# Performance work log

Measured on AMD Instinct MI355X. Metric: run time of the kernel, lower is better.

## Reference

```python
import jax, jax.numpy as jnp
import numpy as np

NUM_HEADS = 16

def setup_inputs() -> dict:
    key = jax.random.key(0)
    k1, k2, k3 = jax.random.split(key, 3)
    B, N, C = 2, 2048, 1024
    x = jax.random.normal(k1, (B, N, C), dtype=jnp.float32)
    w_qkv = jax.random.normal(k2, (C, 3 * C), dtype=jnp.float32) * (C ** -0.5)
    w_proj = jax.random.normal(k3, (C, C), dtype=jnp.float32) * (C ** -0.5)
    b_proj = jnp.zeros((C,), dtype=jnp.float32)
    return {"x": x, "w_qkv": w_qkv, "w_proj": w_proj, "b_proj": b_proj}

def reference(x, w_qkv, w_proj, b_proj):
    B, N, C = x.shape
    H = NUM_HEADS
    D = C // H
    scale = D ** -0.5
    qkv = (x @ w_qkv).reshape(B, N, 3, H, D).transpose(2, 0, 3, 1, 4)  # [3,B,H,N,D]
    q, k, v = qkv[0], qkv[1], qkv[2]
    attn = jnp.einsum("bhnd,bhmd->bhnm", q, k) * scale  # [B,H,N,N]
    attn = jax.nn.softmax(attn, axis=-1)
    out = jnp.einsum("bhnm,bhmd->bhnd", attn, v)  # [B,H,N,D]
    out = out.transpose(0, 2, 1, 3).reshape(B, N, C)
    return out @ w_proj + b_proj
```

## Files before the change

kernel.cpp:

```cpp
#include <hip/hip_runtime.h>
#include <hip/hip_bf16.h>
#include <math.h>

#define B_SZ   2
#define N_SEQ  2048
#define C_DIM  1024
#define H_NUM  16
#define D_HEAD 64
#define M_ROWS (B_SZ * N_SEQ)
#define QKV_N  (3 * C_DIM)

typedef __attribute__((ext_vector_type(8))) short  bf16x8;
typedef __attribute__((ext_vector_type(4))) float  floatx4;

static __device__ __forceinline__ unsigned short f2bf(float x) {
    unsigned int u = __float_as_uint(x);
    u = (u + 0x7FFFu + ((u >> 16) & 1u)) >> 16;
    return (unsigned short)u;
}
static __device__ __forceinline__ unsigned int f2bf_hi(float x) {
    unsigned int u = __float_as_uint(x);
    return u + 0x7FFFu + ((u >> 16) & 1u);
}
#if __has_builtin(__builtin_amdgcn_cvt_pk_bf16_f32)
typedef __bf16 bf16_2 __attribute__((ext_vector_type(2)));
static __device__ __forceinline__ unsigned int pkbf(float a, float b) {
    union { bf16_2 v; unsigned int u; } c;
    c.v = __builtin_amdgcn_cvt_pk_bf16_f32(a, b);
    return c.u;
}
#else
static __device__ __forceinline__ unsigned int pkbf(float a, float b) {
    return __builtin_amdgcn_perm(f2bf_hi(b), f2bf_hi(a), 0x07060302u);
}
#endif

#if __has_builtin(__builtin_amdgcn_exp2f)
#define EXP2F(x) __builtin_amdgcn_exp2f(x)
#else
#define EXP2F(x) exp2f(x)
#endif

#define GLP(p) ((const __attribute__((address_space(1))) void*)(p))
#define LDP(p) ((__attribute__((address_space(3))) void*)(p))

#define CEXP 0.18033688011112042f

__global__ __launch_bounds__(256)
void prep_fused(const float* __restrict__ x,      unsigned short* __restrict__ xb,
                const float* __restrict__ w_qkv,  unsigned short* __restrict__ wqkvT,
                const float* __restrict__ w_proj, unsigned short* __restrict__ wprojT)
{
    __shared__ unsigned short t[64][72];
    const int bid = blockIdx.x;
    const int tid = threadIdx.x;

    if (bid < 4096) {
        const int i = bid * 256 + tid;
        float4 v = ((const float4*)x)[i];
        ushort4 p;
        p.x = f2bf(v.x); p.y = f2bf(v.y); p.z = f2bf(v.z); p.w = f2bf(v.w);
        ((ushort4*)xb)[i] = p;
        return;
    }

    const float* W;
    unsigned short* WT;
    int N, tt;
    if (bid < 4096 + 768) { W = w_qkv;  WT = wqkvT;  N = QKV_N; tt = bid - 4096; }
    else                  { W = w_proj; WT = wprojT; N = C_DIM; tt = bid - 4864; }
    const int ntiles = N / 64;
    const int n0 = (tt % ntiles) * 64;
    const int k0 = (tt / ntiles) * 64;
    const int K  = C_DIM;

    const int tc = tid & 15;
    const int tr = tid >> 4;
    #pragma unroll
    for (int p = 0; p < 4; ++p) {
        const int r = tr + p * 16;
        float4 v = *(const float4*)&W[(size_t)(k0 + r) * N + n0 + tc * 4];
        ushort4 pk;
        pk.x = f2bf(v.x); pk.y = f2bf(v.y); pk.z = f2bf(v.z); pk.w = f2bf(v.w);
        *(ushort4*)&t[r][tc * 4] = pk;
    }
    __syncthreads();

    const int n  = tid >> 2;
    const int c0 = (tid & 3) * 16;
    unsigned short tmp[16];
    #pragma unroll
    for (int i = 0; i < 16; ++i) tmp[i] = t[c0 + i][n];
    *(uint4*)&WT[(size_t)(n0 + n) * K + k0 + c0]     = *(uint4*)&tmp[0];
    *(uint4*)&WT[(size_t)(n0 + n) * K + k0 + c0 + 8] = *(uint4*)&tmp[8];
}

__global__ __launch_bounds__(256)
void gemm_qkv(const unsigned short* __restrict__ A,
              const unsigned short* __restrict__ BT,
              unsigned short* __restrict__ qbuf,
              unsigned short* __restrict__ kbuf,
              unsigned short* __restrict__ vbuf)
{
    const int K = C_DIM;
    __shared__ unsigned short As[128 * 64];
    __shared__ unsigned short Bs[128 * 64];

    const int tid  = threadIdx.x;
    const int lane = tid & 63;
    const int wave = tid >> 6;
    const int l15  = lane & 15;
    const int lq   = lane >> 4;
    const int e7   = l15 & 7;
    const int wm   = (wave & 1) * 64;
    const int wn   = (wave >> 1) * 64;

    const int bid = blockIdx.x;
    const int xcd = bid & 7;
    const int j   = bid >> 3;
    const int bm  = (j / 3) * 128;
    const int bn  = ((j % 3) * 8 + xcd) * 128;

    const int srow = tid >> 3;
    const int gso  = ((tid & 7) ^ (srow & 7)) * 8;

    const unsigned short* ga = A  + (size_t)(bm + srow) * K + gso;
    const unsigned short* gb = BT + (size_t)(bn + srow) * K + gso;

    floatx4 acc[4][4];
    #pragma unroll
    for (int i = 0; i < 4; ++i)
        #pragma unroll
        for (int jj = 0; jj < 4; ++jj) acc[i][jj] = (floatx4){0.f, 0.f, 0.f, 0.f};

    for (int kt = 0; kt < K; kt += 64) {
        #pragma unroll
        for (int i = 0; i < 4; ++i) {
            __builtin_amdgcn_global_load_lds(GLP(ga + (size_t)i * 32 * K + kt),
                                             LDP(&As[i * 2048 + tid * 8]), 16, 0, 0);
            __builtin_amdgcn_global_load_lds(GLP(gb + (size_t)i * 32 * K + kt),
                                             LDP(&Bs[i * 2048 + tid * 8]), 16, 0, 0);
        }
        __syncthreads();

        bf16x8 af[2][4], bfr[2][4];
        #pragma unroll
        for (int t = 0; t < 4; ++t) {
            #pragma unroll
            for (int kc = 0; kc < 2; ++kc) {
                af[kc][t]  = *(const bf16x8*)&As[(wm + t * 16 + l15) * 64
                                                 + (((kc * 4 + lq) ^ e7) * 8)];
                bfr[kc][t] = *(const bf16x8*)&Bs[(wn + t * 16 + l15) * 64
                                                 + (((kc * 4 + lq) ^ e7) * 8)];
            }
        }
        #pragma unroll
        for (int kc = 0; kc < 2; ++kc)
            #pragma unroll
            for (int mt = 0; mt < 4; ++mt)
                #pragma unroll
                for (int nt = 0; nt < 4; ++nt)
                    acc[mt][nt] = __builtin_amdgcn_mfma_f32_16x16x32_bf16(
                        af[kc][mt], bfr[kc][nt], acc[mt][nt], 0, 0, 0);
        __syncthreads();
    }

    #pragma unroll
    for (int nt = 0; nt < 4; ++nt) {
        const int col  = bn + wn + nt * 16 + l15;
        const int reg3 = col >> 10;
        const int h    = (col >> 6) & 15;
        const int d    = col & 63;
        const float sc4 = (reg3 == 0) ? CEXP : 1.0f;
        #pragma unroll
        for (int mt = 0; mt < 4; ++mt) {
            const int row = bm + wm + mt * 16 + lq * 4;
            const int b   = row >> 11;
            const int n   = row & 2047;
            if (reg3 < 2) {
                unsigned short* dst = (reg3 ? kbuf : qbuf)
                    + ((size_t)(b * H_NUM + h) * N_SEQ + n) * D_HEAD + d;
                #pragma unroll
                for (int r = 0; r < 4; ++r)
                    dst[(size_t)r * D_HEAD] = f2bf(acc[mt][nt][r] * sc4);
            } else {
                const int a  = n & 63;
                const int fk = (a & 0x20) | ((a & 0x0C) << 1) | ((a & 0x10) >> 2);
                unsigned short* dst = vbuf
                    + ((size_t)(b * H_NUM + h) * D_HEAD + d) * N_SEQ + (n & ~63) + fk;
                ushort4 pk;
                pk.x = f2bf(acc[mt][nt][0]); pk.y = f2bf(acc[mt][nt][1]);
                pk.z = f2bf(acc[mt][nt][2]); pk.w = f2bf(acc[mt][nt][3]);
                *(ushort4*)dst = pk;
            }
        }
    }
}

__global__ __launch_bounds__(512)
void attn_mfma(const unsigned short* __restrict__ qbuf,
               const unsigned short* __restrict__ kbuf,
               const unsigned short* __restrict__ vbuf,
               unsigned short* __restrict__ attnb)
{
    __shared__ unsigned short KsS[2][64 * 64];
    __shared__ unsigned short VtS[2][64 * 64];

    const int tid  = threadIdx.x;
    const int lane = tid & 63;
    const int wave = tid >> 6;
    const int l15  = lane & 15;
    const int lq   = lane >> 4;
    const int e    = l15 & 7;

    const int bid  = blockIdx.x;
    const int bh   = (bid & 7) * 4 + (bid >> 7);
    const int qblk = (bid >> 3) & 15;
    const int b    = bh >> 4;
    const int h    = bh & 15;
    const int q0   = qblk * 128 + wave * 16;

    const unsigned short* khead = kbuf + (size_t)bh * N_SEQ * D_HEAD;
    const unsigned short* vhead = vbuf + (size_t)bh * D_HEAD * N_SEQ;

    bf16x8 qf[2];
    {
        const unsigned short* qrow = qbuf
            + ((size_t)bh * N_SEQ + q0 + l15) * D_HEAD + lq * 8;
        qf[0] = *(const bf16x8*)qrow;
        qf[1] = *(const bf16x8*)(qrow + 32);
    }

    floatx4 acc[4];
    #pragma unroll
    for (int dc = 0; dc < 4; ++dc) acc[dc] = (floatx4){0.f, 0.f, 0.f, 0.f};
    float lsum = 0.f;

    const int srow = tid >> 3;
    const int gso  = ((tid & 7) ^ (srow & 7)) * 8;

    __builtin_amdgcn_global_load_lds(GLP(khead + (size_t)srow * 64 + gso),
                                     LDP(&KsS[0][tid * 8]), 16, 0, 0);
    __builtin_amdgcn_global_load_lds(GLP(vhead + (size_t)srow * N_SEQ + gso),
                                     LDP(&VtS[0][tid * 8]), 16, 0, 0);

    for (int tile = 0; tile < N_SEQ / 64; ++tile) {
        const int cur = tile & 1;
        __syncthreads();

        if (tile + 1 < N_SEQ / 64) {
            const int m1 = (tile + 1) * 64;
            const int nx = cur ^ 1;
            __builtin_amdgcn_global_load_lds(GLP(khead + (size_t)(m1 + srow) * 64 + gso),
                                             LDP(&KsS[nx][tid * 8]), 16, 0, 0);
            __builtin_amdgcn_global_load_lds(GLP(vhead + (size_t)srow * N_SEQ + m1 + gso),
                                             LDP(&VtS[nx][tid * 8]), 16, 0, 0);
        }

        const unsigned short* Ksc = &KsS[cur][0];
        const unsigned short* Vtc = &VtS[cur][0];

        floatx4 st[4];
        #pragma unroll
        for (int t = 0; t < 4; ++t) {
            bf16x8 k0 = *(const bf16x8*)&Ksc[(t * 16 + l15) * 64 + ((lq ^ e) * 8)];
            bf16x8 k1 = *(const bf16x8*)&Ksc[(t * 16 + l15) * 64 + (((4 + lq) ^ e) * 8)];
            floatx4 s = (floatx4){-8.f, -8.f, -8.f, -8.f};
            s = __builtin_amdgcn_mfma_f32_16x16x32_bf16(k0, qf[0], s, 0, 0, 0);
            s = __builtin_amdgcn_mfma_f32_16x16x32_bf16(k1, qf[1], s, 0, 0, 0);
            st[t] = s;
        }

        unsigned int pk[8];
        float la = 0.f;
        #pragma unroll
        for (int t = 0; t < 4; ++t) {
            float p0 = EXP2F(st[t][0]);
            float p1 = EXP2F(st[t][1]);
            float p2 = EXP2F(st[t][2]);
            float p3 = EXP2F(st[t][3]);
            la += (p0 + p1) + (p2 + p3);
            pk[t * 2]     = pkbf(p0, p1);
            pk[t * 2 + 1] = pkbf(p2, p3);
        }
        lsum += la;
        union { uint4 u; bf16x8 v; } cvt0, cvt1;
        cvt0.u = make_uint4(pk[0], pk[1], pk[2], pk[3]);
        cvt1.u = make_uint4(pk[4], pk[5], pk[6], pk[7]);

        #pragma unroll
        for (int dc = 0; dc < 4; ++dc) {
            bf16x8 v0 = *(const bf16x8*)&Vtc[(dc * 16 + l15) * 64 + ((lq ^ e) * 8)];
            bf16x8 v1 = *(const bf16x8*)&Vtc[(dc * 16 + l15) * 64 + (((4 + lq) ^ e) * 8)];
            acc[dc] = __builtin_amdgcn_mfma_f32_16x16x32_bf16(v0, cvt0.v, acc[dc], 0, 0, 0);
            acc[dc] = __builtin_amdgcn_mfma_f32_16x16x32_bf16(v1, cvt1.v, acc[dc], 0, 0, 0);
        }
    }

    float l = lsum;
    l += __shfl_xor(l, 16, 64);
    l += __shfl_xor(l, 32, 64);
    const float inv = 1.f / l;
    const int q = q0 + l15;
    unsigned short* orow = attnb + ((size_t)b * N_SEQ + q) * C_DIM + h * D_HEAD;
    #pragma unroll
    for (int dc = 0; dc < 4; ++dc) {
        ushort4 pkk;
        pkk.x = f2bf(acc[dc][0] * inv);
        pkk.y = f2bf(acc[dc][1] * inv);
        pkk.z = f2bf(acc[dc][2] * inv);
        pkk.w = f2bf(acc[dc][3] * inv);
        *(ushort4*)&orow[dc * 16 + lq * 4] = pkk;
    }
}

__global__ __launch_bounds__(256)
void gemm_bt(const unsigned short* __restrict__ A,
             const unsigned short* __restrict__ BT,
             const float* __restrict__ bias,
             float* __restrict__ Cm,
             int M, int N, int K)
{
    __shared__ unsigned short As[128 * 64];
    __shared__ unsigned short Bs[64 * 64];

    const int tid  = threadIdx.x;
    const int lane = tid & 63;
    const int wave = tid >> 6;
    const int l15  = lane & 15;
    const int lq   = lane >> 4;
    const int e7   = l15 & 7;
    const int wm   = (wave & 1) * 64;
    const int wn   = (wave >> 1) * 32;

    const int bid = blockIdx.x;
    const int xcd = bid & 7;
    const int j   = bid >> 3;
    const int bm  = (j >> 1) * 128;
    const int bn  = ((j & 1) * 8 + xcd) * 64;

    const int srow = tid >> 3;
    const int gso  = ((tid & 7) ^ (srow & 7)) * 8;

    const unsigned short* ga = A  + (size_t)(bm + srow) * K + gso;
    const unsigned short* gb = BT + (size_t)(bn + srow) * K + gso;

    floatx4 acc[4][2];
    #pragma unroll
    for (int i = 0; i < 4; ++i)
        #pragma unroll
        for (int jj = 0; jj < 2; ++jj) acc[i][jj] = (floatx4){0.f, 0.f, 0.f, 0.f};

    for (int kt = 0; kt < K; kt += 64) {
        #pragma unroll
        for (int i = 0; i < 4; ++i)
            __builtin_amdgcn_global_load_lds(GLP(ga + (size_t)i * 32 * K + kt),
                                             LDP(&As[i * 2048 + tid * 8]), 16, 0, 0);
        #pragma unroll
        for (int i = 0; i < 2; ++i)
            __builtin_amdgcn_global_load_lds(GLP(gb + (size_t)i * 32 * K + kt),
                                             LDP(&Bs[i * 2048 + tid * 8]), 16, 0, 0);
        __syncthreads();

        bf16x8 af[2][4], bfr[2][2];
        #pragma unroll
        for (int t = 0; t < 4; ++t)
            #pragma unroll
            for (int kc = 0; kc < 2; ++kc)
                af[kc][t] = *(const bf16x8*)&As[(wm + t * 16 + l15) * 64
                                                + (((kc * 4 + lq) ^ e7) * 8)];
        #pragma unroll
        for (int t = 0; t < 2; ++t)
            #pragma unroll
            for (int kc = 0; kc < 2; ++kc)
                bfr[kc][t] = *(const bf16x8*)&Bs[(wn + t * 16 + l15) * 64
                                                 + (((kc * 4 + lq) ^ e7) * 8)];
        #pragma unroll
        for (int kc = 0; kc < 2; ++kc)
            #pragma unroll
            for (int mt = 0; mt < 4; ++mt)
                #pragma unroll
                for (int nt = 0; nt < 2; ++nt)
                    acc[mt][nt] = __builtin_amdgcn_mfma_f32_16x16x32_bf16(
                        af[kc][mt], bfr[kc][nt], acc[mt][nt], 0, 0, 0);
        __syncthreads();
    }

    float bv[2];
    #pragma unroll
    for (int nt = 0; nt < 2; ++nt) bv[nt] = bias[bn + wn + nt * 16 + l15];
    #pragma unroll
    for (int mt = 0; mt < 4; ++mt) {
        const int row = bm + wm + mt * 16 + lq * 4;
        #pragma unroll
        for (int nt = 0; nt < 2; ++nt) {
            const int col = bn + wn + nt * 16 + l15;
            #pragma unroll
            for (int r = 0; r < 4; ++r)
                Cm[(size_t)(row + r) * N + col] = acc[mt][nt][r] + bv[nt];
        }
    }
}

extern "C" void kernel_launch(void* const* d_in, const int* in_sizes, int n_in,
                              void* d_out, int out_size, void* d_ws, size_t ws_size,
                              hipStream_t stream)
{
    const float* x      = (const float*)d_in[0];
    const float* w_qkv  = (const float*)d_in[1];
    const float* w_proj = (const float*)d_in[2];
    const float* b_proj = (const float*)d_in[3];
    float*       out    = (float*)d_out;

    unsigned short* xb     = (unsigned short*)d_ws;
    unsigned short* wqkvT  = xb     + (size_t)M_ROWS * C_DIM;
    unsigned short* wprojT = wqkvT  + (size_t)QKV_N * C_DIM;
    unsigned short* qbuf   = wprojT + (size_t)C_DIM * C_DIM;
    unsigned short* kbuf   = qbuf   + (size_t)M_ROWS * C_DIM;
    unsigned short* vbuf   = kbuf   + (size_t)M_ROWS * C_DIM;
    unsigned short* attnb  = vbuf   + (size_t)M_ROWS * C_DIM;

    prep_fused<<<4096 + 768 + 256, 256, 0, stream>>>(x, xb, w_qkv, wqkvT, w_proj, wprojT);

    gemm_qkv<<<768, 256, 0, stream>>>(xb, wqkvT, qbuf, kbuf, vbuf);

    attn_mfma<<<512, 512, 0, stream>>>(qbuf, kbuf, vbuf, attnb);

    gemm_bt<<<512, 256, 0, stream>>>(attnb, wprojT, b_proj, out, M_ROWS, C_DIM, C_DIM);
}
```

Baseline: 191.4 us.

## Process two 16-row query blocks per wave in attention, halving block size

Each wave now handles 32 query rows as two 16-row sub-blocks instead of 16. The K and V fragments read from LDS are reused across both sub-blocks, and the block shrinks from 512 to 256 threads. The two cooperative tile loads now issue twice per thread. The aim is to halve LDS read traffic per MFMA and improve reuse, at the cost of more accumulator registers per thread and fewer waves per block.

```diff
diff --git a/kernel.cpp b/kernel.cpp
--- a/kernel.cpp
+++ b/kernel.cpp
@@ -197,7 +197,7 @@
     }
 }
 
-__global__ __launch_bounds__(512)
+__global__ __launch_bounds__(256)
 void attn_mfma(const unsigned short* __restrict__ qbuf,
                const unsigned short* __restrict__ kbuf,
                const unsigned short* __restrict__ vbuf,
@@ -218,31 +218,37 @@
     const int qblk = (bid >> 3) & 15;
     const int b    = bh >> 4;
     const int h    = bh & 15;
-    const int q0   = qblk * 128 + wave * 16;
+    const int q0   = qblk * 128 + wave * 32;
 
     const unsigned short* khead = kbuf + (size_t)bh * N_SEQ * D_HEAD;
     const unsigned short* vhead = vbuf + (size_t)bh * D_HEAD * N_SEQ;
 
-    bf16x8 qf[2];
-    {
+    bf16x8 qf[2][2];
+    #pragma unroll
+    for (int qb = 0; qb < 2; ++qb) {
         const unsigned short* qrow = qbuf
-            + ((size_t)bh * N_SEQ + q0 + l15) * D_HEAD + lq * 8;
-        qf[0] = *(const bf16x8*)qrow;
-        qf[1] = *(const bf16x8*)(qrow + 32);
-    }
-
-    floatx4 acc[4];
-    #pragma unroll
-    for (int dc = 0; dc < 4; ++dc) acc[dc] = (floatx4){0.f, 0.f, 0.f, 0.f};
-    float lsum = 0.f;
+            + ((size_t)bh * N_SEQ + q0 + qb * 16 + l15) * D_HEAD + lq * 8;
+        qf[0][qb] = *(const bf16x8*)qrow;
+        qf[1][qb] = *(const bf16x8*)(qrow + 32);
+    }
+
+    floatx4 acc[4][2];
+    #pragma unroll
+    for (int dc = 0; dc < 4; ++dc)
+        #pragma unroll
+        for (int qb = 0; qb < 2; ++qb) acc[dc][qb] = (floatx4){0.f, 0.f, 0.f, 0.f};
+    float lsum[2] = {0.f, 0.f};
 
     const int srow = tid >> 3;
     const int gso  = ((tid & 7) ^ (srow & 7)) * 8;
 
-    __builtin_amdgcn_global_load_lds(GLP(khead + (size_t)srow * 64 + gso),
-                                     LDP(&KsS[0][tid * 8]), 16, 0, 0);
-    __builtin_amdgcn_global_load_lds(GLP(vhead + (size_t)srow * N_SEQ + gso),
-                                     LDP(&VtS[0][tid * 8]), 16, 0, 0);
+    #pragma unroll
+    for (int i = 0; i < 2; ++i) {
+        __builtin_amdgcn_global_load_lds(GLP(khead + (size_t)(i * 32 + srow) * 64 + gso),
+                                         LDP(&KsS[0][i * 2048 + tid * 8]), 16, 0, 0);
+        __builtin_amdgcn_global_load_lds(GLP(vhead + (size_t)(i * 32 + srow) * N_SEQ + gso),
+                                         LDP(&VtS[0][i * 2048 + tid * 8]), 16, 0, 0);
+    }
 
     for (int tile = 0; tile < N_SEQ / 64; ++tile) {
         const int cur = tile & 1;
@@ -251,66 +257,88 @@
         if (tile + 1 < N_SEQ / 64) {
             const int m1 = (tile + 1) * 64;
             const int nx = cur ^ 1;
-            __builtin_amdgcn_global_load_lds(GLP(khead + (size_t)(m1 + srow) * 64 + gso),
-                                             LDP(&KsS[nx][tid * 8]), 16, 0, 0);
-            __builtin_amdgcn_global_load_lds(GLP(vhead + (size_t)srow * N_SEQ + m1 + gso),
-                                             LDP(&VtS[nx][tid * 8]), 16, 0, 0);
+            #pragma unroll
+            for (int i = 0; i < 2; ++i) {
+                __builtin_amdgcn_global_load_lds(
+                    GLP(khead + (size_t)(m1 + i * 32 + srow) * 64 + gso),
+                    LDP(&KsS[nx][i * 2048 + tid * 8]), 16, 0, 0);
+                __builtin_amdgcn_global_load_lds(
+                    GLP(vhead + (size_t)(i * 32 + srow) * N_SEQ + m1 + gso),
+                    LDP(&VtS[nx][i * 2048 + tid * 8]), 16, 0, 0);
+            }
         }
 
         const unsigned short* Ksc = &KsS[cur][0];
         const unsigned short* Vtc = &VtS[cur][0];
 
-        floatx4 st[4];
+        floatx4 st[4][2];
         #pragma unroll
         for (int t = 0; t < 4; ++t) {
             bf16x8 k0 = *(const bf16x8*)&Ksc[(t * 16 + l15) * 64 + ((lq ^ e) * 8)];
             bf16x8 k1 = *(const bf16x8*)&Ksc[(t * 16 + l15) * 64 + (((4 + lq) ^ e) * 8)];
-            floatx4 s = (floatx4){-8.f, -8.f, -8.f, -8.f};
-            s = __builtin_amdgcn_mfma_f32_16x16x32_bf16(k0, qf[0], s, 0, 0, 0);
-            s = __builtin_amdgcn_mfma_f32_16x16x32_bf16(k1, qf[1], s, 0, 0, 0);
-            st[t] = s;
-        }
-
-        unsigned int pk[8];
-        float la = 0.f;
-        #pragma unroll
-        for (int t = 0; t < 4; ++t) {
-            float p0 = EXP2F(st[t][0]);
-            float p1 = EXP2F(st[t][1]);
-            float p2 = EXP2F(st[t][2]);
-            float p3 = EXP2F(st[t][3]);
-            la += (p0 + p1) + (p2 + p3);
-            pk[t * 2]     = pkbf(p0, p1);
-            pk[t * 2 + 1] = pkbf(p2, p3);
-        }
-        lsum += la;
-        union { uint4 u; bf16x8 v; } cvt0, cvt1;
-        cvt0.u = make_uint4(pk[0], pk[1], pk[2], pk[3]);
-        cvt1.u = make_uint4(pk[4], pk[5], pk[6], pk[7]);
+            #pragma unroll
+            for (int qb = 0; qb < 2; ++qb) {
+                floatx4 s = (floatx4){-8.f, -8.f, -8.f, -8.f};
+                s = __builtin_amdgcn_mfma_f32_16x16x32_bf16(k0, qf[0][qb], s, 0, 0, 0);
+                s = __builtin_amdgcn_mfma_f32_16x16x32_bf16(k1, qf[1][qb], s, 0, 0, 0);
+                st[t][qb] = s;
+            }
+        }
+
+        bf16x8 pf[2][2];
+        #pragma unroll
+        for (int qb = 0; qb < 2; ++qb) {
+            unsigned int pk[8];
+            float la = 0.f;
+            #pragma unroll
+            for (int t = 0; t < 4; ++t) {
+                float p0 = EXP2F(st[t][qb][0]);
+                float p1 = EXP2F(st[t][qb][1]);
+                float p2 = EXP2F(st[t][qb][2]);
+                float p3 = EXP2F(st[t][qb][3]);
+                la += (p0 + p1) + (p2 + p3);
+                pk[t * 2]     = pkbf(p0, p1);
+                pk[t * 2 + 1] = pkbf(p2, p3);
+            }
+            lsum[qb] += la;
+            union { uint4 u; bf16x8 v; } c0, c1;
+            c0.u = make_uint4(pk[0], pk[1], pk[2], pk[3]);
+            c1.u = make_uint4(pk[4], pk[5], pk[6], pk[7]);
+            pf[0][qb] = c0.v;
+            pf[1][qb] = c1.v;
+        }
 
         #pragma unroll
         for (int dc = 0; dc < 4; ++dc) {
             bf16x8 v0 = *(const bf16x8*)&Vtc[(dc * 16 + l15) * 64 + ((lq ^ e) * 8)];
             bf16x8 v1 = *(const bf16x8*)&Vtc[(dc * 16 + l15) * 64 + (((4 + lq) ^ e) * 8)];
-            acc[dc] = __builtin_amdgcn_mfma_f32_16x16x32_bf16(v0, cvt0.v, acc[dc], 0, 0, 0);
-            acc[dc] = __builtin_amdgcn_mfma_f32_16x16x32_bf16(v1, cvt1.v, acc[dc], 0, 0, 0);
-        }
-    }
-
-    float l = lsum;
-    l += __shfl_xor(l, 16, 64);
-    l += __shfl_xor(l, 32, 64);
-    const float inv = 1.f / l;
-    const int q = q0 + l15;
-    unsigned short* orow = attnb + ((size_t)b * N_SEQ + q) * C_DIM + h * D_HEAD;
-    #pragma unroll
-    for (int dc = 0; dc < 4; ++dc) {
-        ushort4 pkk;
-        pkk.x = f2bf(acc[dc][0] * inv);
-        pkk.y = f2bf(acc[dc][1] * inv);
-        pkk.z = f2bf(acc[dc][2] * inv);
-        pkk.w = f2bf(acc[dc][3] * inv);
-        *(ushort4*)&orow[dc * 16 + lq * 4] = pkk;
+            #pragma unroll
+            for (int qb = 0; qb < 2; ++qb) {
+                acc[dc][qb] = __builtin_amdgcn_mfma_f32_16x16x32_bf16(
+                    v0, pf[0][qb], acc[dc][qb], 0, 0, 0);
+                acc[dc][qb] = __builtin_amdgcn_mfma_f32_16x16x32_bf16(
+                    v1, pf[1][qb], acc[dc][qb], 0, 0, 0);
+            }
+        }
+    }
+
+    #pragma unroll
+    for (int qb = 0; qb < 2; ++qb) {
+        float l = lsum[qb];
+        l += __shfl_xor(l, 16, 64);
+        l += __shfl_xor(l, 32, 64);
+        const float inv = 1.f / l;
+        const int q = q0 + qb * 16 + l15;
+        unsigned short* orow = attnb + ((size_t)b * N_SEQ + q) * C_DIM + h * D_HEAD;
+        #pragma unroll
+        for (int dc = 0; dc < 4; ++dc) {
+            ushort4 pkk;
+            pkk.x = f2bf(acc[dc][qb][0] * inv);
+            pkk.y = f2bf(acc[dc][qb][1] * inv);
+            pkk.z = f2bf(acc[dc][qb][2] * inv);
+            pkk.w = f2bf(acc[dc][qb][3] * inv);
+            *(ushort4*)&orow[dc * 16 + lq * 4] = pkk;
+        }
     }
 }
 
@@ -424,7 +452,7 @@
 
     gemm_qkv<<<768, 256, 0, stream>>>(xb, wqkvT, qbuf, kbuf, vbuf);
 
-    attn_mfma<<<512, 512, 0, stream>>>(qbuf, kbuf, vbuf, attnb);
+    attn_mfma<<<512, 256, 0, stream>>>(qbuf, kbuf, vbuf, attnb);
 
     gemm_bt<<<512, 256, 0, stream>>>(attnb, wprojT, b_proj, out, M_ROWS, C_DIM, C_DIM);
 }
```

Result: slower. 198.4 us (+3.7%).
